# Performance work log

Measured on AMD Instinct MI355X. Metric: run time of the kernel, lower is better.

The kernel has to match this reference:

```python
import jax, jax.numpy as jnp
import numpy as np

TOP_K = 8
NUM_EXPERTS = 64
IN_FEATURES = 4096
TOKENS = 16384


def setup_inputs() -> dict:
    key = jax.random.key(0)
    kx, kw, kb = jax.random.split(key, 3)
    x = jax.random.normal(kx, (TOKENS, IN_FEATURES), dtype=jnp.float32)
    # nn.Linear(in_features, num_experts): W [E, D], b [E]
    bound = 1.0 / np.sqrt(IN_FEATURES)
    W = jax.random.uniform(kw, (NUM_EXPERTS, IN_FEATURES), dtype=jnp.float32, minval=-bound, maxval=bound)
    b = jax.random.uniform(kb, (NUM_EXPERTS,), dtype=jnp.float32, minval=-bound, maxval=bound)
    return {"x": x, "W": W, "b": b}


def reference(x, W, b):
    # gate logits: [T, E]
    logits = jnp.einsum('td,ed->te', x, W) + b
    scores = jax.nn.softmax(logits, axis=-1)
    # top-k per token: [T, K]
    vals, idx = jax.lax.top_k(scores, TOP_K)
    # faithful to torch.sum(expert_values): normalize by GLOBAL sum over all tokens
    weights = vals / jnp.sum(vals)
    return (idx.reshape(-1), weights)
```

## Files before the change

kernel.cpp:

```cpp
#include <hip/hip_runtime.h>
#include <math.h>

typedef float f4 __attribute__((ext_vector_type(4)));

#define TOKENS 16384
#define DIM 4096
#define NE 64
#define KTOP 8
#define BM 64
#define BK 64
#define NT 256
#define NBLK (TOKENS / BM)

__global__ __launch_bounds__(NT) void gate_topk_kernel(
    const float* __restrict__ x, const float* __restrict__ W,
    const float* __restrict__ bias, float* __restrict__ idx_out,
    float* __restrict__ val_out, float* __restrict__ blocksums)
{
    __shared__ float As[BK * BM];
    __shared__ float Bs[BK * NE];
    __shared__ float Ls[BM][NE + 1];

    const int tid = threadIdx.x;
    const int kq = tid & 15;
    const int mg = tid >> 4;
    const int tx = tid & 15;
    const int ty = tid >> 4;
    const int tm = ty << 2;
    const int tn = tx << 2;
    const int row0 = blockIdx.x * BM;

    float bj[4];
#pragma unroll
    for (int j = 0; j < 4; ++j) bj[j] = bias[tn + j];

    const float* xa0 = x + (size_t)(row0 + mg) * DIM + (kq << 2);
    const float* wb0 = W + (size_t)mg * DIM + (kq << 2);

    float acc[4][4] = {};
    f4 fa[4], fb[4];
#pragma unroll
    for (int s = 0; s < 4; ++s) {
        fa[s] = *(const f4*)(xa0 + (size_t)(16 * s) * DIM);
        fb[s] = *(const f4*)(wb0 + (size_t)(16 * s) * DIM);
    }

    for (int kt = 0; kt < DIM / BK; ++kt) {
        __syncthreads();
#pragma unroll
        for (int s = 0; s < 4; ++s) {
            const int m = mg + (s << 4);
            const int c4 = ((m >> 2) ^ kq) & 15;
            const int base = (kq << 2) * BM + (c4 << 2) + (m & 3);
#pragma unroll
            for (int j = 0; j < 4; ++j) {
                As[base + (j << 6)] = fa[s][j];
                Bs[base + (j << 6)] = fb[s][j];
            }
        }
        __syncthreads();
        if (kt + 1 < DIM / BK) {
            const int ko = (kt + 1) * BK;
#pragma unroll
            for (int s = 0; s < 4; ++s) {
                fa[s] = *(const f4*)(xa0 + (size_t)(16 * s) * DIM + ko);
                fb[s] = *(const f4*)(wb0 + (size_t)(16 * s) * DIM + ko);
            }
        }
        float acct[4][4] = {};
#pragma unroll
        for (int kk = 0; kk < BK; ++kk) {
            const int kq2 = kk >> 2;
            const f4 a4 = *(const f4*)&As[kk * BM + (((ty ^ kq2) & 15) << 2)];
            const f4 b4 = *(const f4*)&Bs[kk * NE + (((tx ^ kq2) & 15) << 2)];
#pragma unroll
            for (int i = 0; i < 4; ++i)
#pragma unroll
                for (int j = 0; j < 4; ++j)
                    acct[i][j] = fmaf(a4[i], b4[j], acct[i][j]);
        }
#pragma unroll
        for (int i = 0; i < 4; ++i)
#pragma unroll
            for (int j = 0; j < 4; ++j)
                acc[i][j] += acct[i][j];
    }

#pragma unroll
    for (int i = 0; i < 4; ++i)
#pragma unroll
        for (int j = 0; j < 4; ++j)
            Ls[tm + i][tn + j] = acc[i][j] + bj[j];
    __syncthreads();

    float lsum = 0.0f;
    if (tid < BM) {
        const int m = tid;
        const int token = row0 + m;
        float mx = -INFINITY;
        for (int e = 0; e < NE; ++e) mx = fmaxf(mx, Ls[m][e]);
        float sum = 0.0f;
        for (int e = 0; e < NE; ++e) {
            float p = expf(Ls[m][e] - mx);
            Ls[m][e] = p;
            sum += p;
        }
#pragma unroll
        for (int j = 0; j < KTOP; ++j) {
            float best = -1.0f; int be = 0;
            for (int e = 0; e < NE; ++e) {
                float v = Ls[m][e];
                if (v > best) { best = v; be = e; }
            }
            Ls[m][be] = -1.0f;
            const float val = best / sum;
            idx_out[token * KTOP + j] = (float)be;
            val_out[token * KTOP + j] = val;
            lsum += val;
        }
    }
    if (tid < 64) {
#pragma unroll
        for (int off = 32; off > 0; off >>= 1)
            lsum += __shfl_down(lsum, off, 64);
        if (tid == 0) blocksums[blockIdx.x] = lsum;
    }
}

__global__ __launch_bounds__(256) void scale_kernel(
    const float* __restrict__ blocksums, float* __restrict__ vals)
{
    float total = 0.0f;
    for (int i = 0; i < NBLK; ++i) total += blocksums[i];
    const int i = blockIdx.x * blockDim.x + threadIdx.x;
    vals[i] = vals[i] / total;
}

extern "C" void kernel_launch(void* const* d_in, const int* in_sizes, int n_in,
                              void* d_out, int out_size, void* d_ws, size_t ws_size,
                              hipStream_t stream)
{
    const float* x = (const float*)d_in[0];
    const float* W = (const float*)d_in[1];
    const float* b = (const float*)d_in[2];
    float* idx_out = (float*)d_out;
    float* val_out = idx_out + (size_t)TOKENS * KTOP;
    float* blocksums = (float*)d_ws;

    gate_topk_kernel<<<NBLK, NT, 0, stream>>>(x, W, b, idx_out, val_out, blocksums);
    scale_kernel<<<(TOKENS * KTOP) / 256, 256, 0, stream>>>(blocksums, val_out);
}
```

Baseline: 172.4 us.

## Split-K across four thread groups and parallelize softmax/top-k with wave shuffles

Each block now uses 1024 threads in four groups, each handling a quarter of the K dimension with its own shared-memory tiles, and the partial logits are summed in shared memory. Softmax and top-k move from one serial thread per token to a full 64-lane wave per token using xor-shuffle reductions. The goal is more memory-level parallelism per block and removing the serial epilogue tail. In exchange, shared memory per block grows and occupancy per CU may be limited.

```diff
diff --git a/kernel.cpp b/kernel.cpp
--- a/kernel.cpp
+++ b/kernel.cpp
@@ -4,38 +4,42 @@
 typedef float f4 __attribute__((ext_vector_type(4)));
 
 #define TOKENS 16384
-#define DIM 4096
-#define NE 64
-#define KTOP 8
-#define BM 64
-#define BK 64
-#define NT 256
-#define NBLK (TOKENS / BM)
+#define DIM    4096
+#define NE     64
+#define KTOP   8
+#define BM     64
+#define BK     64
+#define NGRP   4
+#define KRANGE (DIM / NGRP)
+#define NTILE  (KRANGE / BK)
+#define NT     1024
+#define NBLK   (TOKENS / BM)
 
-__global__ __launch_bounds__(NT) void gate_topk_kernel(
+__global__ __launch_bounds__(NT, 4) void gate_topk_kernel(
     const float* __restrict__ x, const float* __restrict__ W,
     const float* __restrict__ bias, float* __restrict__ idx_out,
     float* __restrict__ val_out, float* __restrict__ blocksums)
 {
-    __shared__ float As[BK * BM];
-    __shared__ float Bs[BK * NE];
-    __shared__ float Ls[BM][NE + 1];
+    __shared__ float smem[NGRP][2][BK * BM];
+    __shared__ float bsum[16];
 
     const int tid = threadIdx.x;
-    const int kq = tid & 15;
-    const int mg = tid >> 4;
-    const int tx = tid & 15;
-    const int ty = tid >> 4;
+    const int g   = tid >> 8;
+    const int gt  = tid & 255;
+    const int kq = gt & 15;
+    const int mg = gt >> 4;
+    const int tx = gt & 15;
+    const int ty = gt >> 4;
     const int tm = ty << 2;
     const int tn = tx << 2;
     const int row0 = blockIdx.x * BM;
 
-    float bj[4];
-#pragma unroll
-    for (int j = 0; j < 4; ++j) bj[j] = bias[tn + j];
+    float* As = smem[g][0];
+    float* Bs = smem[g][1];
 
-    const float* xa0 = x + (size_t)(row0 + mg) * DIM + (kq << 2);
-    const float* wb0 = W + (size_t)mg * DIM + (kq << 2);
+    const int kbase = g * KRANGE;
+    const float* xa0 = x + (size_t)(row0 + mg) * DIM + kbase + (kq << 2);
+    const float* wb0 = W + (size_t)mg * DIM + kbase + (kq << 2);
 
     float acc[4][4] = {};
     f4 fa[4], fb[4];
@@ -45,11 +49,11 @@
         fb[s] = *(const f4*)(wb0 + (size_t)(16 * s) * DIM);
     }
 
-    for (int kt = 0; kt < DIM / BK; ++kt) {
+    for (int kt = 0; kt < NTILE; ++kt) {
         __syncthreads();
 #pragma unroll
         for (int s = 0; s < 4; ++s) {
-            const int m = mg + (s << 4);
+            const int m  = mg + (s << 4);
             const int c4 = ((m >> 2) ^ kq) & 15;
             const int base = (kq << 2) * BM + (c4 << 2) + (m & 3);
 #pragma unroll
@@ -59,7 +63,7 @@
             }
         }
         __syncthreads();
-        if (kt + 1 < DIM / BK) {
+        if (kt + 1 < NTILE) {
             const int ko = (kt + 1) * BK;
 #pragma unroll
             for (int s = 0; s < 4; ++s) {
@@ -86,44 +90,61 @@
                 acc[i][j] += acct[i][j];
     }
 
-#pragma unroll
-    for (int i = 0; i < 4; ++i)
-#pragma unroll
-        for (int j = 0; j < 4; ++j)
-            Ls[tm + i][tn + j] = acc[i][j] + bj[j];
     __syncthreads();
 
-    float lsum = 0.0f;
-    if (tid < BM) {
-        const int m = tid;
-        const int token = row0 + m;
-        float mx = -INFINITY;
-        for (int e = 0; e < NE; ++e) mx = fmaxf(mx, Ls[m][e]);
-        float sum = 0.0f;
-        for (int e = 0; e < NE; ++e) {
-            float p = expf(Ls[m][e] - mx);
-            Ls[m][e] = p;
-            sum += p;
-        }
+#pragma unroll
+    for (int i = 0; i < 4; ++i) {
+        f4 v = { acc[i][0], acc[i][1], acc[i][2], acc[i][3] };
+        *(f4*)&As[(tm + i) * NE + tn] = v;
+    }
+    __syncthreads();
+
+    const int wv   = tid >> 6;
+    const int lane = tid & 63;
+    const float bv = bias[lane];
+    float wsum = 0.0f;
+#pragma unroll
+    for (int tt = 0; tt < 4; ++tt) {
+        const int t = wv * 4 + tt;
+        const int token = row0 + t;
+        const float logit = smem[0][0][t * NE + lane] + smem[1][0][t * NE + lane]
+                          + smem[2][0][t * NE + lane] + smem[3][0][t * NE + lane] + bv;
+        float mx = logit;
+#pragma unroll
+        for (int off = 32; off > 0; off >>= 1)
+            mx = fmaxf(mx, __shfl_xor(mx, off, 64));
+        const float p = expf(logit - mx);
+        float s = p;
+#pragma unroll
+        for (int off = 32; off > 0; off >>= 1)
+            s += __shfl_xor(s, off, 64);
+        const float rs = 1.0f / s;
+        float pv = p;
 #pragma unroll
         for (int j = 0; j < KTOP; ++j) {
-            float best = -1.0f; int be = 0;
-            for (int e = 0; e < NE; ++e) {
-                float v = Ls[m][e];
-                if (v > best) { best = v; be = e; }
+            float v = pv; int e = lane;
+#pragma unroll
+            for (int off = 1; off < 64; off <<= 1) {
+                const float v2 = __shfl_xor(v, off, 64);
+                const int   e2 = __shfl_xor(e, off, 64);
+                if (v2 > v || (v2 == v && e2 < e)) { v = v2; e = e2; }
             }
-            Ls[m][be] = -1.0f;
-            const float val = best / sum;
-            idx_out[token * KTOP + j] = (float)be;
-            val_out[token * KTOP + j] = val;
-            lsum += val;
+            const float val = v * rs;
+            if (lane == j) {
+                idx_out[token * KTOP + j] = (float)e;
+                val_out[token * KTOP + j] = val;
+            }
+            if (lane == e) pv = -1.0f;
+            wsum += val;
         }
     }
-    if (tid < 64) {
+    if (lane == 0) bsum[wv] = wsum;
+    __syncthreads();
+    if (tid == 0) {
+        float t = 0.0f;
 #pragma unroll
-        for (int off = 32; off > 0; off >>= 1)
-            lsum += __shfl_down(lsum, off, 64);
-        if (tid == 0) blocksums[blockIdx.x] = lsum;
+        for (int i = 0; i < 16; ++i) t += bsum[i];
+        blocksums[blockIdx.x] = t;
     }
 }
 
```

Result: slower. 348.2 us (+102.0%).
